# Optimization experiments

Measured on AMD Instinct MI355X. Metric: run time of the kernel, lower is better.

The kernel has to match this reference:

```python
import jax, jax.numpy as jnp
import numpy as np

B, T, E, H = 4, 1024, 512, 8
DH = E // H  # head dim = 64


def setup_inputs() -> dict:
    key = jax.random.key(0)
    ks = jax.random.split(key, 6)
    s = 1.0 / np.sqrt(E)
    return {
        "q": jax.random.normal(ks[0], (B, T, E), dtype=jnp.float32),
        "kv": jax.random.normal(ks[1], (B, T, E), dtype=jnp.float32),
        "Wq": jax.random.normal(ks[2], (E, E), dtype=jnp.float32) * s,
        "Wk": jax.random.normal(ks[3], (E, E), dtype=jnp.float32) * s,
        "Wv": jax.random.normal(ks[4], (E, E), dtype=jnp.float32) * s,
        "Wo": jax.random.normal(ks[5], (E, E), dtype=jnp.float32) * s,
        "head_num": H,
    }


def _split_heads_dh(x, h):
    # einops 'b t (d h)' with h=head_num: head index is FASTEST in channel dim
    b, t, e = x.shape
    d = e // h
    return x.reshape(b, t, d, h).transpose(0, 3, 1, 2)  # (b, h, t, d)


def reference(q, kv, Wq, Wk, Wv, Wo, head_num):
    e = q.shape[-1]
    dk = (e // head_num) ** 0.5  # NOTE: multiplied, per original code

    qp = q @ Wq   # weights stored as (in, out); Linear(bias=False)
    kp = kv @ Wk
    vp = kv @ Wv

    query = _split_heads_dh(qp, head_num)  # (b, h, t, d)
    key = _split_heads_dh(kp, head_num)
    value = _split_heads_dh(vp, head_num)

    qf = jnp.fft.fftn(query, axes=(-2, -1))  # complex, over (t, d)
    kf = jnp.fft.fftn(key, axes=(-2, -1))

    # complex einsum, key NOT conjugated (faithful to torch source)
    energy = jnp.einsum("bhid,bhjd->bhij", qf, kf) * dk
    energy = jnp.fft.ifftn(energy, axes=(-2, -1)).real  # (b, h, t, t)

    attention = jax.nn.softmax(energy, axis=-1)
    out = jnp.einsum("bhij,bhjd->bhid", attention, value)  # (b, h, t, d)

    # einops 'b h t d -> b t (h d)': head index SLOWEST in output channel dim
    b, h, t, d = out.shape
    out = out.transpose(0, 2, 1, 3).reshape(b, t, h * d)
    return out @ Wo
```

## Files before the change

kernel.cpp:

```cpp
#include <hip/hip_runtime.h>
#include <math.h>

#define BB 4
#define TT 1024
#define EE 512
#define HH 8
#define DD 64
#define BT (BB * TT)

typedef _Float16 f16;
typedef __attribute__((ext_vector_type(8))) _Float16 f16x8;
typedef __attribute__((ext_vector_type(4))) float f32x4;

__device__ __forceinline__ void dma16(const f16* g, char* l) {
    __builtin_amdgcn_global_load_lds(
        (const __attribute__((address_space(1))) void*)g,
        (__attribute__((address_space(3))) void*)l, 16, 0, 0);
}

__global__ __launch_bounds__(256) void prep_k(
    const float* __restrict__ q, const float* __restrict__ kv,
    const float* __restrict__ Wq, const float* __restrict__ Wk,
    const float* __restrict__ Wv, const float* __restrict__ Wo,
    f16* __restrict__ wqh, f16* __restrict__ wql,
    f16* __restrict__ wkh, f16* __restrict__ wkl,
    f16* __restrict__ wvh, f16* __restrict__ woh,
    f16* __restrict__ qAhi, f16* __restrict__ qAlo,
    f16* __restrict__ kvAhi, f16* __restrict__ kvAlo) {
    const int t = threadIdx.x;
    const int y = blockIdx.y;
    if (y < 4) {
        int idx = blockIdx.x * 256 + t;
        int k = idx & (EE - 1);
        int n = idx >> 9;
        if (y == 0) {
            float v = Wq[k * EE + n] * 512.0f;
            f16 hi = (f16)v;
            wqh[n * EE + k] = hi;
            wql[n * EE + k] = (f16)(v - (float)hi);
        } else if (y == 1) {
            int d = n >> 3, h = n & 7;
            int sn = (((DD - d) & (DD - 1)) << 3) | h;
            float v = Wk[k * EE + sn];
            f16 hi = (f16)v;
            wkh[n * EE + k] = hi;
            wkl[n * EE + k] = (f16)(v - (float)hi);
        } else if (y == 2) {
            wvh[n * EE + k] = (f16)Wv[k * EE + n];
        } else {
            woh[n * EE + k] = (f16)Wo[k * EE + n];
        }
    } else {
        const float* src = (y == 4) ? q : kv;
        f16* dh = (y == 4) ? qAhi : kvAhi;
        f16* dl = (y == 4) ? qAlo : kvAlo;
        int base = (blockIdx.x * 256 + t) * 8;
        float4 a = *(const float4*)&src[base];
        float4 c = *(const float4*)&src[base + 4];
        float xs[8] = {a.x, a.y, a.z, a.w, c.x, c.y, c.z, c.w};
        f16x8 hi, lo;
#pragma unroll
        for (int e = 0; e < 8; ++e) {
            f16 hh = (f16)xs[e];
            hi[e] = hh;
            lo[e] = (f16)(xs[e] - (float)hh);
        }
        *(f16x8*)&dh[base] = hi;
        *(f16x8*)&dl[base] = lo;
    }
}

__global__ __launch_bounds__(256) void proj_k(
    const f16* __restrict__ qAhi, const f16* __restrict__ qAlo,
    const f16* __restrict__ kvAhi, const f16* __restrict__ kvAlo,
    const f16* __restrict__ wqh, const f16* __restrict__ wql,
    const f16* __restrict__ wkh, const f16* __restrict__ wkl,
    const f16* __restrict__ wvh,
    f16* __restrict__ qhi, f16* __restrict__ qlo,
    f16* __restrict__ kthi, f16* __restrict__ ktlo, f16* __restrict__ vP) {
    __shared__ __align__(16) f16 A_s[2][2][128][32];
    __shared__ __align__(16) f16 W_s[2][3][64][32];
    f16 (*Ep)[136] = reinterpret_cast<f16(*)[136]>(&A_s[0][0][0][0]);

    const int t = threadIdx.x;
    const int w = t >> 6, l = t & 63;
    const int wm = w >> 1, wn = w & 1;
    const int fr = l & 15, fc = l >> 4;
    const int m0b = blockIdx.x * 128;
    const int n0b = blockIdx.y * 64;
    const int z   = blockIdx.z;

    const f16* AH = z ? kvAhi : qAhi;
    const f16* AL = z ? kvAlo : qAlo;
    const f16* WH = z ? wkh : wqh;
    const f16* WL = z ? wkl : wql;

    f32x4 accK[4][2], accV[4][2];
#pragma unroll
    for (int i = 0; i < 4; ++i)
#pragma unroll
        for (int j = 0; j < 2; ++j) {
            accK[i][j] = f32x4{0.f, 0.f, 0.f, 0.f};
            accV[i][j] = f32x4{0.f, 0.f, 0.f, 0.f};
        }

    auto stageDMA = [&](int bf, int k0) {
#pragma unroll
        for (int i = 0; i < 2; ++i) {
            int slot = (i * 4 + w) * 64 + l;
            int r = slot >> 2, qv = slot & 3;
            const f16* gh = AH + (size_t)(m0b + r) * EE + k0 + qv * 8;
            const f16* gl = AL + (size_t)(m0b + r) * EE + k0 + qv * 8;
            dma16(gh, (char*)&A_s[bf][0][0][0] + (i * 4 + w) * 1024);
            dma16(gl, (char*)&A_s[bf][1][0][0] + (i * 4 + w) * 1024);
        }
        {
            int slot = w * 64 + l;
            int r = slot >> 2, qv = slot & 3;
            const f16* g0 = WH + (size_t)(n0b + r) * EE + k0 + qv * 8;
            const f16* g1 = WL + (size_t)(n0b + r) * EE + k0 + qv * 8;
            dma16(g0, (char*)&W_s[bf][0][0][0] + w * 1024);
            dma16(g1, (char*)&W_s[bf][1][0][0] + w * 1024);
            if (z) {
                const f16* g2 = wvh + (size_t)(n0b + r) * EE + k0 + qv * 8;
                dma16(g2, (char*)&W_s[bf][2][0][0] + w * 1024);
            }
        }
    };

    auto comp = [&](int bf) {
        f16x8 Ahf[4], Alf[4], Bh[2], Bl[2], Bv[2];
#pragma unroll
        for (int mi = 0; mi < 4; ++mi) {
            Ahf[mi] = *(const f16x8*)&A_s[bf][0][wm * 64 + mi * 16 + fr][fc * 8];
            Alf[mi] = *(const f16x8*)&A_s[bf][1][wm * 64 + mi * 16 + fr][fc * 8];
        }
#pragma unroll
        for (int nj = 0; nj < 2; ++nj) {
            Bh[nj] = *(const f16x8*)&W_s[bf][0][wn * 32 + nj * 16 + fr][fc * 8];
            Bl[nj] = *(const f16x8*)&W_s[bf][1][wn * 32 + nj * 16 + fr][fc * 8];
            if (z) Bv[nj] = *(const f16x8*)&W_s[bf][2][wn * 32 + nj * 16 + fr][fc * 8];
        }
        __builtin_amdgcn_s_setprio(1);
#pragma unroll
        for (int mi = 0; mi < 4; ++mi)
#pragma unroll
            for (int nj = 0; nj < 2; ++nj) {
                accK[mi][nj] = __builtin_amdgcn_mfma_f32_16x16x32_f16(
                    Ahf[mi], Bh[nj], accK[mi][nj], 0, 0, 0);
                accK[mi][nj] = __builtin_amdgcn_mfma_f32_16x16x32_f16(
                    Ahf[mi], Bl[nj], accK[mi][nj], 0, 0, 0);
                accK[mi][nj] = __builtin_amdgcn_mfma_f32_16x16x32_f16(
                    Alf[mi], Bh[nj], accK[mi][nj], 0, 0, 0);
                if (z)
                    accV[mi][nj] = __builtin_amdgcn_mfma_f32_16x16x32_f16(
                        Ahf[mi], Bv[nj], accV[mi][nj], 0, 0, 0);
            }
        __builtin_amdgcn_s_setprio(0);
    };

    stageDMA(0, 0);
    __syncthreads();
    int cur = 0;
    for (int ks = 0; ks < 16; ++ks) {
        if (ks < 15) stageDMA(cur ^ 1, (ks + 1) * 32);
        comp(cur);
        __syncthreads();
        cur ^= 1;
    }

    const int d0  = n0b >> 3;
    const int kfc = d0 >> 5;
    const int lg2 = (d0 >> 3) & 3;
#pragma unroll
    for (int mi = 0; mi < 4; ++mi)
#pragma unroll
        for (int nj = 0; nj < 2; ++nj)
#pragma unroll
            for (int r = 0; r < 4; ++r)
                Ep[wn * 32 + nj * 16 + fr][wm * 64 + mi * 16 + fc * 4 + r] =
                    (f16)accK[mi][nj][r];
    __syncthreads();
#pragma unroll
    for (int i = 0; i < 4; ++i) {
        int task = t * 4 + i;
        int mr = task >> 3, h = task & 7;
        f16x8 v;
#pragma unroll
        for (int d = 0; d < 8; ++d) v[d] = Ep[8 * d + h][mr];
        if (z == 0) {
            *(f16x8*)&qhi[((size_t)h * BT + m0b + mr) * DD + d0] = v;
        } else {
            int mg = m0b + mr;
            int bb = mg >> 10, key = mg & 1023;
            size_t off = ((((((size_t)h * BB + bb) * 16 + (key >> 6)) * 4 +
                            ((key >> 4) & 3)) * 2 + kfc) * 64 +
                          lg2 * 16 + (key & 15)) * 8;
            *(f16x8*)&kthi[off] = v;
        }
    }
    __syncthreads();
#pragma unroll
    for (int mi = 0; mi < 4; ++mi)
#pragma unroll
        for (int nj = 0; nj < 2; ++nj)
#pragma unroll
            for (int r = 0; r < 4; ++r) {
                float x = accK[mi][nj][r];
                f16 hh = (f16)x;
                Ep[wn * 32 + nj * 16 + fr][wm * 64 + mi * 16 + fc * 4 + r] =
                    (f16)(x - (float)hh);
            }
    __syncthreads();
#pragma unroll
    for (int i = 0; i < 4; ++i) {
        int task = t * 4 + i;
        int mr = task >> 3, h = task & 7;
        f16x8 v;
#pragma unroll
        for (int d = 0; d < 8; ++d) v[d] = Ep[8 * d + h][mr];
        if (z == 0) {
            *(f16x8*)&qlo[((size_t)h * BT + m0b + mr) * DD + d0] = v;
        } else {
            int mg = m0b + mr;
            int bb = mg >> 10, key = mg & 1023;
            size_t off = ((((((size_t)h * BB + bb) * 16 + (key >> 6)) * 4 +
                            ((key >> 4) & 3)) * 2 + kfc) * 64 +
                          lg2 * 16 + (key & 15)) * 8;
            *(f16x8*)&ktlo[off] = v;
        }
    }
    if (z) {
        __syncthreads();
#pragma unroll
        for (int mi = 0; mi < 4; ++mi)
#pragma unroll
            for (int nj = 0; nj < 2; ++nj)
#pragma unroll
                for (int r = 0; r < 4; ++r)
                    Ep[wn * 32 + nj * 16 + fr][wm * 64 + mi * 16 + fc * 4 + r] =
                        (f16)accV[mi][nj][r];
        __syncthreads();
#pragma unroll
        for (int i = 0; i < 4; ++i) {
            int task = t * 4 + i;
            int mg = task & 15, nn = task >> 4;
            int h = nn & 7, dl = nn >> 3;
            int d = d0 + dl;
            int koff = m0b + mg * 8;
            int tile = koff >> 6;
            int kf   = (koff >> 5) & 1;
            int lgv  = (koff >> 3) & 3;
            int dvt  = d >> 4, lqd = d & 15;
            f16x8 v = *(const f16x8*)&Ep[nn][mg * 8];
            size_t off = (((((size_t)h * 64 + tile) * 2 + kf) * 4 + dvt) * 64 +
                          lgv * 16 + lqd) * 8;
            *(f16x8*)&vP[off] = v;
        }
    }
}

__global__ __launch_bounds__(256) void outmm_k(const f16* __restrict__ Af,
                                               const f16* __restrict__ WThi,
                                               float* __restrict__ out) {
    __shared__ __align__(16) f16 Ah_s[2][64][72];
    __shared__ __align__(16) f16 Wh_s[2][64][72];

    const int t = threadIdx.x;
    const int w = t >> 6, l = t & 63;
    const int wm = w >> 1, wn = w & 1;
    const int fr = l & 15, fc = l >> 4;
    const int m0b = blockIdx.x * 64;
    const int n0b = blockIdx.y * 64;
    const int sr = t >> 2, sch = t & 3;

    f32x4 acc[2][2];
#pragma unroll
    for (int i = 0; i < 2; ++i)
#pragma unroll
        for (int j = 0; j < 2; ++j) acc[i][j] = f32x4{0.f, 0.f, 0.f, 0.f};

    f16x8 af[2], wf[2];
    auto loadAB = [&](int k0) {
#pragma unroll
        for (int i = 0; i < 2; ++i) {
            af[i] = *(const f16x8*)&Af[(size_t)(m0b + sr) * EE + k0 + sch * 16 + i * 8];
            wf[i] = *(const f16x8*)&WThi[(size_t)(n0b + sr) * EE + k0 + sch * 16 + i * 8];
        }
    };
    auto stage = [&](int bf) {
#pragma unroll
        for (int i = 0; i < 2; ++i) {
            *(f16x8*)&Ah_s[bf][sr][sch * 16 + i * 8] = af[i];
            *(f16x8*)&Wh_s[bf][sr][sch * 16 + i * 8] = wf[i];
        }
    };

    loadAB(0);
    stage(0);
    __syncthreads();
    int cur = 0;
    for (int ks = 0; ks < 8; ++ks) {
        if (ks < 7) loadAB((ks + 1) * 64);
        f16x8 Ahf[2][2], Bhf[2][2];
#pragma unroll
        for (int mi = 0; mi < 2; ++mi)
#pragma unroll
            for (int kb = 0; kb < 2; ++kb)
                Ahf[mi][kb] =
                    *(const f16x8*)&Ah_s[cur][wm * 32 + mi * 16 + fr][kb * 32 + fc * 8];
#pragma unroll
        for (int nj = 0; nj < 2; ++nj)
#pragma unroll
            for (int kb = 0; kb < 2; ++kb)
                Bhf[nj][kb] =
                    *(const f16x8*)&Wh_s[cur][wn * 32 + nj * 16 + fr][kb * 32 + fc * 8];
        __builtin_amdgcn_s_setprio(1);
#pragma unroll
        for (int mi = 0; mi < 2; ++mi)
#pragma unroll
            for (int nj = 0; nj < 2; ++nj)
#pragma unroll
                for (int kb = 0; kb < 2; ++kb)
                    acc[mi][nj] = __builtin_amdgcn_mfma_f32_16x16x32_f16(
                        Ahf[mi][kb], Bhf[nj][kb], acc[mi][nj], 0, 0, 0);
        __builtin_amdgcn_s_setprio(0);
        if (ks < 7) stage(cur ^ 1);
        __syncthreads();
        cur ^= 1;
    }

#pragma unroll
    for (int mi = 0; mi < 2; ++mi)
#pragma unroll
        for (int nj = 0; nj < 2; ++nj)
#pragma unroll
            for (int r = 0; r < 4; ++r)
                out[(size_t)(m0b + wm * 32 + mi * 16 + fc * 4 + r) * EE +
                    n0b + wn * 32 + nj * 16 + fr] = acc[mi][nj][r];
}

__global__ __launch_bounds__(512) void attn_mfma_k(const f16* __restrict__ qhiP,
    const f16* __restrict__ qloP, const f16* __restrict__ kthiP,
    const f16* __restrict__ ktloP, const f16* __restrict__ vP,
    f16* __restrict__ ctx) {
    __shared__ __align__(16) f16 KhiL[2][4096];
    __shared__ __align__(16) f16 KloL[2][4096];
    __shared__ __align__(16) f16 VL[2][4096];
    __shared__ __align__(16) f16 Pl[8][16][88];

    const int bid = blockIdx.x;
    const int bx = (bid >> 3) & 7;
    const int h  = bid & 7;
    const int b  = bid >> 6;

    const int t  = threadIdx.x;
    const int w  = t >> 6;
    const int l  = t & 63;
    const int lg = l >> 4;
    const int lq = l & 15;
    const int q0 = bx * 128 + w * 16;
    const size_t plane = ((size_t)h * BT + (size_t)b * TT) * DD;

    f16x8 Qhi[2], Qlo[2];
#pragma unroll
    for (int kf = 0; kf < 2; ++kf) {
        size_t qo = plane + (size_t)(q0 + lq) * DD + kf * 32 + lg * 8;
        Qhi[kf] = *(const f16x8*)&qhiP[qo];
        Qlo[kf] = *(const f16x8*)&qloP[qo];
    }

    f32x4 Oacc[4];
#pragma unroll
    for (int i = 0; i < 4; ++i) Oacc[i] = f32x4{0.f, 0.f, 0.f, 0.f};
    float m = -1e30f, lsum = 0.f;

    const f16* khb = kthiP + (((size_t)h * BB + b) << 16);
    const f16* klb = ktloP + (((size_t)h * BB + b) << 16);
    const f16* vtb = vP + ((size_t)h * 64 + b * 16) * 4096;

    auto stageDMA = [&](int bf, int tile) {
        const f16* ks = khb + (size_t)tile * 4096 + t * 8;
        const f16* ls = klb + (size_t)tile * 4096 + t * 8;
        const f16* vs = vtb + (size_t)tile * 4096 + t * 8;
        dma16(ks, (char*)&KhiL[bf][0] + w * 1024);
        dma16(ls, (char*)&KloL[bf][0] + w * 1024);
        dma16(vs, (char*)&VL[bf][0] + w * 1024);
    };

    auto QK1 = [&](int bf, int kt) -> f32x4 {
        const f16* bh = &KhiL[bf][kt * 1024];
        const f16* bl = &KloL[bf][kt * 1024];
        f16x8 s0 = *(const f16x8*)&bh[l * 8];
        f16x8 s1 = *(const f16x8*)&bh[512 + l * 8];
        f16x8 s2 = *(const f16x8*)&bl[l * 8];
        f16x8 s3 = *(const f16x8*)&bl[512 + l * 8];
        f32x4 c = f32x4{0.f, 0.f, 0.f, 0.f};
        __builtin_amdgcn_s_setprio(1);
        c = __builtin_amdgcn_mfma_f32_16x16x32_f16(s0, Qhi[0], c, 0, 0, 0);
        c = __builtin_amdgcn_mfma_f32_16x16x32_f16(s0, Qlo[0], c, 0, 0, 0);
        c = __builtin_amdgcn_mfma_f32_16x16x32_f16(s2, Qhi[0], c, 0, 0, 0);
        c = __builtin_amdgcn_mfma_f32_16x16x32_f16(s1, Qhi[1], c, 0, 0, 0);
        c = __builtin_amdgcn_mfma_f32_16x16x32_f16(s1, Qlo[1], c, 0, 0, 0);
        c = __builtin_amdgcn_mfma_f32_16x16x32_f16(s3, Qhi[1], c, 0, 0, 0);
        __builtin_amdgcn_s_setprio(0);
        return c;
    };

    auto SMPV = [&](int bf, const f32x4 (&Sc)[4]) {
        float sv[16];
#pragma unroll
        for (int kt = 0; kt < 4; ++kt)
#pragma unroll
            for (int r = 0; r < 4; ++r) sv[kt * 4 + r] = Sc[kt][r];
        float tm = sv[0];
#pragma unroll
        for (int i = 1; i < 16; ++i) tm = fmaxf(tm, sv[i]);
        tm = fmaxf(tm, __shfl_xor(tm, 16));
        tm = fmaxf(tm, __shfl_xor(tm, 32));

        bool skip = __all(tm <= m + 8.0f);
        float Mn = m, corr = 1.0f;
        if (!skip) {
            Mn = fmaxf(m, tm);
            corr = __expf(m - Mn);
        }
        float ps = 0.f;
        f16 ph[16];
#pragma unroll
        for (int i = 0; i < 16; ++i) {
            float p = __expf(sv[i] - Mn);
            ps += p;
            ph[i] = (f16)p;
        }
        ps += __shfl_xor(ps, 16);
        ps += __shfl_xor(ps, 32);
        if (skip) {
            lsum += ps;
        } else {
            lsum = lsum * corr + ps;
            m = Mn;
        }

#pragma unroll
        for (int kt = 0; kt < 4; ++kt)
#pragma unroll
            for (int rp = 0; rp < 4; rp += 2) {
                union { f16 h; unsigned short u; } u0, u1;
                u0.h = ph[kt * 4 + rp]; u1.h = ph[kt * 4 + rp + 1];
                unsigned int pk = ((unsigned int)u1.u << 16) | u0.u;
                *(unsigned int*)&Pl[w][lq][kt * 16 + lg * 4 + rp] = pk;
            }

        if (!skip) {
            float cq[4];
#pragma unroll
            for (int r = 0; r < 4; ++r) cq[r] = __shfl(corr, lg * 4 + r);
#pragma unroll
            for (int dvt = 0; dvt < 4; ++dvt)
#pragma unroll
                for (int r = 0; r < 4; ++r) Oacc[dvt][r] *= cq[r];
        }

        __builtin_amdgcn_s_setprio(1);
#pragma unroll
        for (int kf = 0; kf < 2; ++kf) {
            f16x8 pa = *(const f16x8*)&Pl[w][lq][kf * 32 + lg * 8];
#pragma unroll
            for (int dvt = 0; dvt < 4; ++dvt) {
                f16x8 bv = *(const f16x8*)&VL[bf][((kf * 4 + dvt) * 64 + l) * 8];
                Oacc[dvt] = __builtin_amdgcn_mfma_f32_16x16x32_f16(
                    pa, bv, Oacc[dvt], 0, 0, 0);
            }
        }
        __builtin_amdgcn_s_setprio(0);
    };

    stageDMA(0, 0);
    __syncthreads();
    int cur = 0;
    for (int tile = 0; tile < 16; ++tile) {
        if (tile + 1 < 16) stageDMA(cur ^ 1, tile + 1);
        f32x4 Sc[4];
#pragma unroll
        for (int kt = 0; kt < 4; ++kt) Sc[kt] = QK1(cur, kt);
        SMPV(cur, Sc);
        __syncthreads();
        cur ^= 1;
    }

    float linv = 1.0f / lsum;
    float lq4[4];
#pragma unroll
    for (int r = 0; r < 4; ++r) lq4[r] = __shfl(linv, lg * 4 + r);
#pragma unroll
    for (int r = 0; r < 4; ++r) {
        f16* crow = ctx + (size_t)(b * TT + q0 + lg * 4 + r) * EE + h * DD;
#pragma unroll
        for (int dvt = 0; dvt < 4; ++dvt)
            crow[dvt * 16 + lq] = (f16)(Oacc[dvt][r] * lq4[r]);
    }
}

extern "C" void kernel_launch(void* const* d_in, const int* in_sizes, int n_in,
                              void* d_out, int out_size, void* d_ws, size_t ws_size,
                              hipStream_t stream) {
    const float* q  = (const float*)d_in[0];
    const float* kv = (const float*)d_in[1];
    const float* Wq = (const float*)d_in[2];
    const float* Wk = (const float*)d_in[3];
    const float* Wv = (const float*)d_in[4];
    const float* Wo = (const float*)d_in[5];
    float* out = (float*)d_out;

    f16* ws = (f16*)d_ws;
    const size_t PL  = (size_t)HH * BT * DD;
    const size_t WPL = (size_t)EE * EE;
    f16* qhi   = ws + 0 * PL;
    f16* qlo   = ws + 1 * PL;
    f16* kthi  = ws + 2 * PL;
    f16* ktlo  = ws + 3 * PL;
    f16* vPck  = ws + 4 * PL;
    f16* ctx   = ws + 5 * PL;
    f16* qAhi  = ws + 6 * PL;
    f16* qAlo  = ws + 7 * PL;
    f16* kvAhi = ws + 8 * PL;
    f16* kvAlo = ws + 9 * PL;
    f16* wqh = ws + 10 * PL;
    f16* wql = wqh + 1 * WPL;
    f16* wkh = wqh + 2 * WPL;
    f16* wkl = wqh + 3 * WPL;
    f16* wvh = wqh + 4 * WPL;
    f16* woh = wqh + 5 * WPL;

    prep_k<<<dim3(1024, 6), dim3(256), 0, stream>>>(
        q, kv, Wq, Wk, Wv, Wo, wqh, wql, wkh, wkl, wvh, woh,
        qAhi, qAlo, kvAhi, kvAlo);

    proj_k<<<dim3(BT / 128, EE / 64, 2), dim3(256), 0, stream>>>(
        qAhi, qAlo, kvAhi, kvAlo, wqh, wql, wkh, wkl, wvh,
        qhi, qlo, kthi, ktlo, vPck);

    attn_mfma_k<<<dim3(256), dim3(512), 0, stream>>>(
        qhi, qlo, kthi, ktlo, vPck, ctx);

    outmm_k<<<dim3(BT / 64, EE / 64), dim3(256), 0, stream>>>(ctx, woh, out);
}
```

Before: 75.64 us.

## Switch attention kernel to 32x32x16 MFMA with 32 query rows per wave

The attention kernel now uses four waves per block, each handling 32 query rows with 32x32x16 MFMA instructions instead of eight waves of 16 rows with 16x16x32. This halves the LDS reads of K/V per query row and reduces softmax shuffle reductions, since more of each row lives in registers. The cost is fewer waves per block for latency hiding, higher register pressure from the 16-wide accumulators, and a more intricate P/V layout that has to match the larger MFMA operand mapping.

```diff
diff --git a/kernel.cpp b/kernel.cpp
--- a/kernel.cpp
+++ b/kernel.cpp
@@ -11,6 +11,7 @@
 typedef _Float16 f16;
 typedef __attribute__((ext_vector_type(8))) _Float16 f16x8;
 typedef __attribute__((ext_vector_type(4))) float f32x4;
+typedef __attribute__((ext_vector_type(16))) float f32x16;
 
 __device__ __forceinline__ void dma16(const f16* g, char* l) {
     __builtin_amdgcn_global_load_lds(
@@ -340,14 +341,14 @@
                     n0b + wn * 32 + nj * 16 + fr] = acc[mi][nj][r];
 }
 
-__global__ __launch_bounds__(512) void attn_mfma_k(const f16* __restrict__ qhiP,
+__global__ __launch_bounds__(256) void attn_mfma_k(const f16* __restrict__ qhiP,
     const f16* __restrict__ qloP, const f16* __restrict__ kthiP,
     const f16* __restrict__ ktloP, const f16* __restrict__ vP,
     f16* __restrict__ ctx) {
     __shared__ __align__(16) f16 KhiL[2][4096];
     __shared__ __align__(16) f16 KloL[2][4096];
     __shared__ __align__(16) f16 VL[2][4096];
-    __shared__ __align__(16) f16 Pl[8][16][88];
+    __shared__ __align__(16) f16 Pl[4][32][72];
 
     const int bid = blockIdx.x;
     const int bx = (bid >> 3) & 7;
@@ -357,22 +358,25 @@
     const int t  = threadIdx.x;
     const int w  = t >> 6;
     const int l  = t & 63;
-    const int lg = l >> 4;
-    const int lq = l & 15;
-    const int q0 = bx * 128 + w * 16;
+    const int lh = l >> 5;
+    const int lq = l & 31;
+    const int l16 = l & 15;
+    const int q0 = bx * 128 + w * 32;
     const size_t plane = ((size_t)h * BT + (size_t)b * TT) * DD;
 
-    f16x8 Qhi[2], Qlo[2];
-#pragma unroll
-    for (int kf = 0; kf < 2; ++kf) {
-        size_t qo = plane + (size_t)(q0 + lq) * DD + kf * 32 + lg * 8;
-        Qhi[kf] = *(const f16x8*)&qhiP[qo];
-        Qlo[kf] = *(const f16x8*)&qloP[qo];
-    }
-
-    f32x4 Oacc[4];
-#pragma unroll
-    for (int i = 0; i < 4; ++i) Oacc[i] = f32x4{0.f, 0.f, 0.f, 0.f};
+    f16x8 Qhi[4], Qlo[4];
+#pragma unroll
+    for (int dw = 0; dw < 4; ++dw) {
+        size_t qo = plane + (size_t)(q0 + lq) * DD + dw * 16 + lh * 8;
+        Qhi[dw] = *(const f16x8*)&qhiP[qo];
+        Qlo[dw] = *(const f16x8*)&qloP[qo];
+    }
+
+    f32x16 Oacc[2];
+#pragma unroll
+    for (int i = 0; i < 2; ++i)
+#pragma unroll
+        for (int r = 0; r < 16; ++r) Oacc[i][r] = 0.f;
     float m = -1e30f, lsum = 0.f;
 
     const f16* khb = kthiP + (((size_t)h * BB + b) << 16);
@@ -380,44 +384,49 @@
     const f16* vtb = vP + ((size_t)h * 64 + b * 16) * 4096;
 
     auto stageDMA = [&](int bf, int tile) {
-        const f16* ks = khb + (size_t)tile * 4096 + t * 8;
-        const f16* ls = klb + (size_t)tile * 4096 + t * 8;
-        const f16* vs = vtb + (size_t)tile * 4096 + t * 8;
-        dma16(ks, (char*)&KhiL[bf][0] + w * 1024);
-        dma16(ls, (char*)&KloL[bf][0] + w * 1024);
-        dma16(vs, (char*)&VL[bf][0] + w * 1024);
-    };
-
-    auto QK1 = [&](int bf, int kt) -> f32x4 {
-        const f16* bh = &KhiL[bf][kt * 1024];
-        const f16* bl = &KloL[bf][kt * 1024];
-        f16x8 s0 = *(const f16x8*)&bh[l * 8];
-        f16x8 s1 = *(const f16x8*)&bh[512 + l * 8];
-        f16x8 s2 = *(const f16x8*)&bl[l * 8];
-        f16x8 s3 = *(const f16x8*)&bl[512 + l * 8];
-        f32x4 c = f32x4{0.f, 0.f, 0.f, 0.f};
+#pragma unroll
+        for (int i = 0; i < 2; ++i) {
+            const f16* ks = khb + (size_t)tile * 4096 + (i * 256 + t) * 8;
+            const f16* ls = klb + (size_t)tile * 4096 + (i * 256 + t) * 8;
+            const f16* vs = vtb + (size_t)tile * 4096 + (i * 256 + t) * 8;
+            dma16(ks, (char*)&KhiL[bf][0] + (i * 4 + w) * 1024);
+            dma16(ls, (char*)&KloL[bf][0] + (i * 4 + w) * 1024);
+            dma16(vs, (char*)&VL[bf][0] + (i * 4 + w) * 1024);
+        }
+    };
+
+    auto QK32 = [&](int bf, int kb) -> f32x16 {
+        f32x16 c;
+#pragma unroll
+        for (int r = 0; r < 16; ++r) c[r] = 0.f;
+        const int kt = kb * 2 + (lq >> 4);
         __builtin_amdgcn_s_setprio(1);
-        c = __builtin_amdgcn_mfma_f32_16x16x32_f16(s0, Qhi[0], c, 0, 0, 0);
-        c = __builtin_amdgcn_mfma_f32_16x16x32_f16(s0, Qlo[0], c, 0, 0, 0);
-        c = __builtin_amdgcn_mfma_f32_16x16x32_f16(s2, Qhi[0], c, 0, 0, 0);
-        c = __builtin_amdgcn_mfma_f32_16x16x32_f16(s1, Qhi[1], c, 0, 0, 0);
-        c = __builtin_amdgcn_mfma_f32_16x16x32_f16(s1, Qlo[1], c, 0, 0, 0);
-        c = __builtin_amdgcn_mfma_f32_16x16x32_f16(s3, Qhi[1], c, 0, 0, 0);
+#pragma unroll
+        for (int dw = 0; dw < 4; ++dw) {
+            int kf = dw >> 1, lg = (dw & 1) * 2 + lh;
+            int off = ((kt * 2 + kf) * 64 + lg * 16 + l16) * 8;
+            f16x8 shi = *(const f16x8*)&KhiL[bf][off];
+            f16x8 slo = *(const f16x8*)&KloL[bf][off];
+            c = __builtin_amdgcn_mfma_f32_32x32x16_f16(shi, Qhi[dw], c, 0, 0, 0);
+            c = __builtin_amdgcn_mfma_f32_32x32x16_f16(shi, Qlo[dw], c, 0, 0, 0);
+            c = __builtin_amdgcn_mfma_f32_32x32x16_f16(slo, Qhi[dw], c, 0, 0, 0);
+        }
         __builtin_amdgcn_s_setprio(0);
         return c;
     };
 
-    auto SMPV = [&](int bf, const f32x4 (&Sc)[4]) {
-        float sv[16];
-#pragma unroll
-        for (int kt = 0; kt < 4; ++kt)
-#pragma unroll
-            for (int r = 0; r < 4; ++r) sv[kt * 4 + r] = Sc[kt][r];
-        float tm = sv[0];
-#pragma unroll
-        for (int i = 1; i < 16; ++i) tm = fmaxf(tm, sv[i]);
-        tm = fmaxf(tm, __shfl_xor(tm, 16));
-        tm = fmaxf(tm, __shfl_xor(tm, 32));
+    auto SMPV = [&](int bf, const f32x16& S0, const f32x16& S1) {
+        float sv[32];
+#pragma unroll
+        for (int r = 0; r < 16; ++r) { sv[r] = S0[r]; sv[16 + r] = S1[r]; }
+        float mx[16];
+#pragma unroll
+        for (int i = 0; i < 16; ++i) mx[i] = fmaxf(sv[i], sv[i + 16]);
+#pragma unroll
+        for (int st = 8; st > 0; st >>= 1)
+#pragma unroll
+            for (int i = 0; i < st; ++i) mx[i] = fmaxf(mx[i], mx[i + st]);
+        float tm = fmaxf(mx[0], __shfl_xor(mx[0], 32));
 
         bool skip = __all(tm <= m + 8.0f);
         float Mn = m, corr = 1.0f;
@@ -425,16 +434,20 @@
             Mn = fmaxf(m, tm);
             corr = __expf(m - Mn);
         }
-        float ps = 0.f;
-        f16 ph[16];
+        f16 ph[32];
+        float sm[16];
 #pragma unroll
         for (int i = 0; i < 16; ++i) {
-            float p = __expf(sv[i] - Mn);
-            ps += p;
-            ph[i] = (f16)p;
-        }
-        ps += __shfl_xor(ps, 16);
-        ps += __shfl_xor(ps, 32);
+            float p0 = __expf(sv[i] - Mn);
+            float p1 = __expf(sv[i + 16] - Mn);
+            ph[i] = (f16)p0; ph[i + 16] = (f16)p1;
+            sm[i] = p0 + p1;
+        }
+#pragma unroll
+        for (int st = 8; st > 0; st >>= 1)
+#pragma unroll
+            for (int i = 0; i < st; ++i) sm[i] += sm[i + st];
+        float ps = sm[0] + __shfl_xor(sm[0], 32);
         if (skip) {
             lsum += ps;
         } else {
@@ -443,34 +456,43 @@
         }
 
 #pragma unroll
-        for (int kt = 0; kt < 4; ++kt)
-#pragma unroll
-            for (int rp = 0; rp < 4; rp += 2) {
-                union { f16 h; unsigned short u; } u0, u1;
-                u0.h = ph[kt * 4 + rp]; u1.h = ph[kt * 4 + rp + 1];
-                unsigned int pk = ((unsigned int)u1.u << 16) | u0.u;
-                *(unsigned int*)&Pl[w][lq][kt * 16 + lg * 4 + rp] = pk;
+        for (int kb = 0; kb < 2; ++kb)
+#pragma unroll
+            for (int rg = 0; rg < 4; ++rg) {
+                int col = kb * 32 + 8 * rg + 4 * lh;
+                int i0 = kb * 16 + rg * 4;
+                union { f16 h2[2]; unsigned int u; } pk0, pk1;
+                pk0.h2[0] = ph[i0];     pk0.h2[1] = ph[i0 + 1];
+                pk1.h2[0] = ph[i0 + 2]; pk1.h2[1] = ph[i0 + 3];
+                *(unsigned int*)&Pl[w][lq][col]     = pk0.u;
+                *(unsigned int*)&Pl[w][lq][col + 2] = pk1.u;
             }
 
         if (!skip) {
-            float cq[4];
-#pragma unroll
-            for (int r = 0; r < 4; ++r) cq[r] = __shfl(corr, lg * 4 + r);
-#pragma unroll
-            for (int dvt = 0; dvt < 4; ++dvt)
-#pragma unroll
-                for (int r = 0; r < 4; ++r) Oacc[dvt][r] *= cq[r];
+            float cq[16];
+#pragma unroll
+            for (int r = 0; r < 16; ++r) {
+                int rowq = (r & 3) + 8 * (r >> 2) + 4 * lh;
+                cq[r] = __shfl(corr, rowq);
+            }
+#pragma unroll
+            for (int db = 0; db < 2; ++db)
+#pragma unroll
+                for (int r = 0; r < 16; ++r) Oacc[db][r] *= cq[r];
         }
 
         __builtin_amdgcn_s_setprio(1);
 #pragma unroll
-        for (int kf = 0; kf < 2; ++kf) {
-            f16x8 pa = *(const f16x8*)&Pl[w][lq][kf * 32 + lg * 8];
-#pragma unroll
-            for (int dvt = 0; dvt < 4; ++dvt) {
-                f16x8 bv = *(const f16x8*)&VL[bf][((kf * 4 + dvt) * 64 + l) * 8];
-                Oacc[dvt] = __builtin_amdgcn_mfma_f32_16x16x32_f16(
-                    pa, bv, Oacc[dvt], 0, 0, 0);
+        for (int kw = 0; kw < 4; ++kw) {
+            f16x8 pa = *(const f16x8*)&Pl[w][lq][kw * 16 + lh * 8];
+            int kf = kw >> 1, lgv = (kw & 1) * 2 + lh;
+#pragma unroll
+            for (int db = 0; db < 2; ++db) {
+                int dvt = db * 2 + (lq >> 4);
+                f16x8 bv = *(const f16x8*)&VL[bf][((kf * 4 + dvt) * 64 +
+                                                   lgv * 16 + l16) * 8];
+                Oacc[db] = __builtin_amdgcn_mfma_f32_32x32x16_f16(
+                    pa, bv, Oacc[db], 0, 0, 0);
             }
         }
         __builtin_amdgcn_s_setprio(0);
@@ -481,24 +503,21 @@
     int cur = 0;
     for (int tile = 0; tile < 16; ++tile) {
         if (tile + 1 < 16) stageDMA(cur ^ 1, tile + 1);
-        f32x4 Sc[4];
-#pragma unroll
-        for (int kt = 0; kt < 4; ++kt) Sc[kt] = QK1(cur, kt);
-        SMPV(cur, Sc);
+        f32x16 S0 = QK32(cur, 0);
+        f32x16 S1 = QK32(cur, 1);
+        SMPV(cur, S0, S1);
         __syncthreads();
         cur ^= 1;
     }
 
     float linv = 1.0f / lsum;
-    float lq4[4];
-#pragma unroll
-    for (int r = 0; r < 4; ++r) lq4[r] = __shfl(linv, lg * 4 + r);
-#pragma unroll
-    for (int r = 0; r < 4; ++r) {
-        f16* crow = ctx + (size_t)(b * TT + q0 + lg * 4 + r) * EE + h * DD;
-#pragma unroll
-        for (int dvt = 0; dvt < 4; ++dvt)
-            crow[dvt * 16 + lq] = (f16)(Oacc[dvt][r] * lq4[r]);
+#pragma unroll
+    for (int r = 0; r < 16; ++r) {
+        int rowq = (r & 3) + 8 * (r >> 2) + 4 * lh;
+        float lv = __shfl(linv, rowq);
+        f16* crow = ctx + (size_t)(b * TT + q0 + rowq) * EE + h * DD;
+        crow[lq]      = (f16)(Oacc[0][r] * lv);
+        crow[32 + lq] = (f16)(Oacc[1][r] * lv);
     }
 }
 
@@ -541,7 +560,7 @@
         qAhi, qAlo, kvAhi, kvAlo, wqh, wql, wkh, wkl, wvh,
         qhi, qlo, kthi, ktlo, vPck);
 
-    attn_mfma_k<<<dim3(256), dim3(512), 0, stream>>>(
+    attn_mfma_k<<<dim3(256), dim3(256), 0, stream>>>(
         qhi, qlo, kthi, ktlo, vPck, ctx);
 
     outmm_k<<<dim3(BT / 64, EE / 64), dim3(256), 0, stream>>>(ctx, woh, out);
```

New measurement: 82.10 us. +8.5%, slower.
